# Optimization experiments

Hardware: AMD Instinct MI355X
Metric: run time of the kernel (lower is better)

## Reference

```python
import jax, jax.numpy as jnp
import numpy as np

N_NODES = 100000
N_GRAPHS = 512
D_IN = 300
D_HID = 300
D_OUT = 128  # 2 * SEQUENCE_LENGTH


def _gcn_norm(edge_index, n):
    # PyG GCNConv default: add self-loops, symmetric normalization
    src, dst = edge_index[0], edge_index[1]
    loop = jnp.arange(n, dtype=src.dtype)
    src = jnp.concatenate([src, loop])
    dst = jnp.concatenate([dst, loop])
    deg = jax.ops.segment_sum(jnp.ones_like(dst, dtype=jnp.float32), dst, num_segments=n)
    dinv = jnp.where(deg > 0, jax.lax.rsqrt(deg), 0.0)
    norm = dinv[src] * dinv[dst]  # [E+N]
    return src, dst, norm


def _gcn_conv(x, src, dst, norm, W, b, n):
    h = x @ W                              # transform first (PyG order)
    msg = norm[:, None] * h[src]           # gather + scale, [E+N, D]
    agg = jax.ops.segment_sum(msg, dst, num_segments=n)  # scatter-add
    return agg + b


def setup_inputs() -> dict:
    key = jax.random.key(0)
    ks = jax.random.split(key, 10)
    x = jax.random.normal(ks[0], (N_NODES, D_IN), dtype=jnp.float32)
    edge_index = jax.random.randint(ks[1], (2, 800000), 0, N_NODES, dtype=jnp.int64)
    batch = jnp.sort(jax.random.randint(ks[2], (N_NODES,), 0, N_GRAPHS, dtype=jnp.int64))
    s = 1.0 / np.sqrt(D_IN)
    W1 = jax.random.uniform(ks[3], (D_IN, D_HID), jnp.float32, -s, s)
    b1 = jnp.zeros((D_HID,), jnp.float32)
    W2 = jax.random.uniform(ks[4], (D_HID, D_HID), jnp.float32, -s, s)
    b2 = jnp.zeros((D_HID,), jnp.float32)
    W3 = jax.random.uniform(ks[5], (D_HID, D_OUT), jnp.float32, -s, s)
    b3 = jnp.zeros((D_OUT,), jnp.float32)
    Wm = jax.random.uniform(ks[6], (D_OUT, 1), jnp.float32, -s, s)
    bm = jnp.zeros((1,), jnp.float32)
    return {"x": x, "edge_index": edge_index, "batch": batch,
            "W1": W1, "b1": b1, "W2": W2, "b2": b2,
            "W3": W3, "b3": b3, "Wm": Wm, "bm": bm}


def reference(x, edge_index, batch, W1, b1, W2, b2, W3, b3, Wm, bm):
    n = x.shape[0]
    src, dst, norm = _gcn_norm(edge_index, n)
    # dropout is identity in eval mode
    h = jax.nn.relu(_gcn_conv(x, src, dst, norm, W1, b1, n))
    h = jax.nn.relu(_gcn_conv(h, src, dst, norm, W2, b2, n))
    h = jax.nn.relu(_gcn_conv(h, src, dst, norm, W3, b3, n))
    # global mean pool over graphs
    sums = jax.ops.segment_sum(h, batch, num_segments=N_GRAPHS)
    cnt = jax.ops.segment_sum(jnp.ones((n,), jnp.float32), batch, num_segments=N_GRAPHS)
    readout = sums / jnp.maximum(cnt, 1.0)[:, None]   # [G, D_OUT]
    return (readout @ Wm + bm)[:, 0]                  # [G]
```

## Files before the change

kernel.cpp:

```cpp
#include <hip/hip_runtime.h>
#include <hip/hip_bf16.h>

typedef __bf16 bf16;
typedef __bf16 bf16x4 __attribute__((ext_vector_type(4)));
typedef __bf16 bf16x8 __attribute__((ext_vector_type(8)));
typedef float f32x4 __attribute__((ext_vector_type(4)));

constexpr int N_NODES  = 100000;
constexpr int N_EDGES  = 800000;
constexpr int N_GRAPHS = 512;
constexpr int D_IN  = 300;
constexpr int D_HID = 300;
constexpr int D_OUT = 128;
constexpr int KP    = 320;
constexpr int MT    = 128;
constexpr int NTILE = (N_NODES + MT - 1) / MT;
constexpr int NPAD  = NTILE * MT;

#define AS1(p) ((const __attribute__((address_space(1))) void*)(p))
#define AS3(p) ((__attribute__((address_space(3))) void*)(p))


__global__ __launch_bounds__(256) void k_init(int* deg, float* gsum, int* cnt) {
  int i = blockIdx.x * 256 + threadIdx.x;
  if (i < N_NODES) deg[i] = 0;
  if (i < N_GRAPHS) { gsum[i] = 0.f; cnt[i] = 0; }
}

__global__ __launch_bounds__(256) void k_deg(const int* __restrict__ ei, int* __restrict__ deg) {
  int e = blockIdx.x * 256 + threadIdx.x;
  if (e < N_EDGES) atomicAdd(&deg[ei[N_EDGES + e]], 1);
}

__global__ __launch_bounds__(256) void k_dinv(const int* __restrict__ deg, float* __restrict__ dinv) {
  int v = blockIdx.x * 256 + threadIdx.x;
  if (v < N_NODES) dinv[v] = rsqrtf((float)(deg[v] + 1));
}

__global__ __launch_bounds__(256) void k_scan1(const int* __restrict__ deg, int* __restrict__ rp,
                                               int* __restrict__ part) {
  __shared__ int sm[256];
  int tid = threadIdx.x;
  int i = blockIdx.x * 256 + tid;
  int v = (i < N_NODES) ? deg[i] : 0;
  sm[tid] = v;
  __syncthreads();
  for (int off = 1; off < 256; off <<= 1) {
    int t = (tid >= off) ? sm[tid - off] : 0;
    __syncthreads();
    sm[tid] += t;
    __syncthreads();
  }
  if (i < N_NODES) rp[i] = sm[tid] - v;
  if (tid == 255) part[blockIdx.x] = sm[255];
}

__global__ __launch_bounds__(512) void k_scan2(int* part, int nb) {
  __shared__ int sm[512];
  int tid = threadIdx.x;
  int v = (tid < nb) ? part[tid] : 0;
  sm[tid] = v;
  __syncthreads();
  for (int off = 1; off < 512; off <<= 1) {
    int t = (tid >= off) ? sm[tid - off] : 0;
    __syncthreads();
    sm[tid] += t;
    __syncthreads();
  }
  if (tid < nb) part[tid] = sm[tid] - v;
}

__global__ __launch_bounds__(256) void k_scan3(int* __restrict__ rp, const int* __restrict__ part,
                                               int* __restrict__ cur) {
  int i = blockIdx.x * 256 + threadIdx.x;
  if (i < N_NODES) {
    int r = rp[i] + part[blockIdx.x];
    rp[i] = r;
    cur[i] = r;
  }
  if (i == 0) rp[N_NODES] = N_EDGES;
}

__global__ __launch_bounds__(256) void k_fill(const int* __restrict__ ei, int* __restrict__ cur,
                                              int* __restrict__ col) {
  int e = blockIdx.x * 256 + threadIdx.x;
  if (e < N_EDGES) {
    int s = ei[e];
    int d = ei[N_EDGES + e];
    int p = atomicAdd(&cur[d], 1);
    col[p] = s;
  }
}


__global__ __launch_bounds__(256) void k_conv_x(const float* __restrict__ x, const float* __restrict__ dinv,
                                                bf16* __restrict__ Xs) {
  int i = blockIdx.x * 256 + threadIdx.x;
  if (i >= N_NODES * (KP / 4)) return;
  int j = i % (KP / 4);
  int v = i / (KP / 4);
  float4 f = make_float4(0.f, 0.f, 0.f, 0.f);
  if (j < D_IN / 4) f = ((const float4*)(x + (size_t)v * D_IN))[j];
  float dv = dinv[v];
  bf16x4 o;
  o[0] = (bf16)(f.x * dv); o[1] = (bf16)(f.y * dv); o[2] = (bf16)(f.z * dv); o[3] = (bf16)(f.w * dv);
  *(bf16x4*)(Xs + (size_t)v * KP + j * 4) = o;
}

__global__ __launch_bounds__(256) void k_conv_w(const float* __restrict__ W, bf16* __restrict__ Wt,
                                                int Kin, int Nin) {
  int i = blockIdx.x * 256 + threadIdx.x;
  if (i >= KP * KP) return;
  int k = i % KP;
  int n = i / KP;
  float f = (k < Kin && n < Nin) ? W[k * Nin + n] : 0.f;
  Wt[i] = (bf16)f;
}


__global__ __launch_bounds__(256) void k_aggb(const bf16* __restrict__ in, const int* __restrict__ rp,
                                              const int* __restrict__ col, const float* __restrict__ dinv,
                                              bf16* __restrict__ out) {
  int w = threadIdx.x >> 6, l = threadIdx.x & 63;
  int v = blockIdx.x * 4 + w;
  if (v >= N_NODES) return;
  if (l >= 40) return;
  const size_t co = (size_t)8 * l;

  float A0[8], A1[8];
  {
    bf16x8 p = *(const bf16x8*)(in + (size_t)v * KP + co);
#pragma unroll
    for (int j = 0; j < 8; ++j) { A0[j] = (float)p[j]; A1[j] = 0.f; }
  }
  int s = rp[v], e = rp[v + 1];
  int i = s;
  for (; i + 8 <= e; i += 8) {
    bf16x8 p0 = *(const bf16x8*)(in + (size_t)col[i]     * KP + co);
    bf16x8 p1 = *(const bf16x8*)(in + (size_t)col[i + 1] * KP + co);
    bf16x8 p2 = *(const bf16x8*)(in + (size_t)col[i + 2] * KP + co);
    bf16x8 p3 = *(const bf16x8*)(in + (size_t)col[i + 3] * KP + co);
    bf16x8 p4 = *(const bf16x8*)(in + (size_t)col[i + 4] * KP + co);
    bf16x8 p5 = *(const bf16x8*)(in + (size_t)col[i + 5] * KP + co);
    bf16x8 p6 = *(const bf16x8*)(in + (size_t)col[i + 6] * KP + co);
    bf16x8 p7 = *(const bf16x8*)(in + (size_t)col[i + 7] * KP + co);
#pragma unroll
    for (int j = 0; j < 8; ++j) {
      A0[j] += ((float)p0[j] + (float)p2[j]) + ((float)p4[j] + (float)p6[j]);
      A1[j] += ((float)p1[j] + (float)p3[j]) + ((float)p5[j] + (float)p7[j]);
    }
  }
  for (; i + 4 <= e; i += 4) {
    bf16x8 p0 = *(const bf16x8*)(in + (size_t)col[i]     * KP + co);
    bf16x8 p1 = *(const bf16x8*)(in + (size_t)col[i + 1] * KP + co);
    bf16x8 p2 = *(const bf16x8*)(in + (size_t)col[i + 2] * KP + co);
    bf16x8 p3 = *(const bf16x8*)(in + (size_t)col[i + 3] * KP + co);
#pragma unroll
    for (int j = 0; j < 8; ++j) {
      A0[j] += (float)p0[j] + (float)p2[j];
      A1[j] += (float)p1[j] + (float)p3[j];
    }
  }
  for (; i + 2 <= e; i += 2) {
    bf16x8 p0 = *(const bf16x8*)(in + (size_t)col[i]     * KP + co);
    bf16x8 p1 = *(const bf16x8*)(in + (size_t)col[i + 1] * KP + co);
#pragma unroll
    for (int j = 0; j < 8; ++j) { A0[j] += (float)p0[j]; A1[j] += (float)p1[j]; }
  }
  if (i < e) {
    bf16x8 p0 = *(const bf16x8*)(in + (size_t)col[i] * KP + co);
#pragma unroll
    for (int j = 0; j < 8; ++j) A0[j] += (float)p0[j];
  }
  float dv = dinv[v];
  bf16x8 o;
#pragma unroll
  for (int j = 0; j < 8; ++j) o[j] = (bf16)((A0[j] + A1[j]) * dv);
  *(bf16x8*)(out + (size_t)v * KP + co) = o;
}


template <int NP, int WM, int WN, bool LAST>
__global__ __launch_bounds__(512, 4) void k_gemm(const bf16* __restrict__ A, const bf16* __restrict__ Bt,
                                                 const float* __restrict__ dinv, const float* __restrict__ bias,
                                                 const float* __restrict__ Wm, bf16* __restrict__ H,
                                                 float* __restrict__ sArr) {
  constexpr int WROWS = MT / WM;
  constexpr int MI    = WROWS / 16;
  constexpr int WCOLS = NP / WN;
  constexpr int NC    = WCOLS / 16;
  constexpr int NB_B  = NP / 64;
  __shared__ __attribute__((aligned(16))) char sA[MT * 128];
  __shared__ __attribute__((aligned(16))) char sB[NP * 128];

  const int tid = threadIdx.x;
  const int w = tid >> 6, l = tid & 63;
  const int wm = w / WN, wn = w % WN;
  const int m0 = blockIdx.x * MT;

  const int sr  = tid >> 3;
  const int ssw = ((tid & 7) << 4) ^ ((sr & 7) << 4);
  const char* Ab = (const char*)A;
  const char* Bb = (const char*)Bt;

  const int la = l & 15, q = l >> 4;
  const int msk = (la & 7) << 4;

  f32x4 acc[MI][NC] = {};

  for (int kh = 0; kh < 5; ++kh) {
#pragma unroll
    for (int i = 0; i < 2; ++i) {
      const char* src = Ab + (size_t)(m0 + i * 64 + sr) * 640 + kh * 128 + ssw;
      __builtin_amdgcn_global_load_lds(AS1(src), AS3(sA + i * 8192 + w * 1024), 16, 0, 0);
    }
#pragma unroll
    for (int i = 0; i < NB_B; ++i) {
      const char* src = Bb + (size_t)(i * 64 + sr) * 640 + kh * 128 + ssw;
      __builtin_amdgcn_global_load_lds(AS1(src), AS3(sB + i * 8192 + w * 1024), 16, 0, 0);
    }
    __syncthreads();

#pragma unroll
    for (int ks = 0; ks < 2; ++ks) {
      const int cb = (ks * 64 + q * 16) ^ msk;
      bf16x8 af[MI];
#pragma unroll
      for (int mi = 0; mi < MI; ++mi) {
        int r = wm * WROWS + mi * 16 + la;
        af[mi] = *(const bf16x8*)(sA + r * 128 + cb);
      }
#pragma unroll
      for (int nc = 0; nc < NC; ++nc) {
        int rb = wn * WCOLS + nc * 16 + la;
        bf16x8 bfr = *(const bf16x8*)(sB + rb * 128 + cb);
#pragma unroll
        for (int mi = 0; mi < MI; ++mi)
          acc[mi][nc] = __builtin_amdgcn_mfma_f32_16x16x32_bf16(af[mi], bfr, acc[mi][nc], 0, 0, 0);
      }
    }
    __syncthreads();
  }

  const int rbase = m0 + wm * WROWS + q * 4;
  if (!LAST) {
    float bc[NC];
#pragma unroll
    for (int nc = 0; nc < NC; ++nc) {
      int c = wn * WCOLS + nc * 16 + la;
      bc[nc] = (c < D_HID) ? bias[c] : 0.f;
    }
#pragma unroll
    for (int mi = 0; mi < MI; ++mi) {
#pragma unroll
      for (int r = 0; r < 4; ++r) {
        int row = rbase + mi * 16 + r;
        if (row < N_NODES) {
          float dv = dinv[row];
#pragma unroll
          for (int nc = 0; nc < NC; ++nc) {
            int c = wn * WCOLS + nc * 16 + la;
            H[(size_t)row * KP + c] = (bf16)(fmaxf(acc[mi][nc][r] + bc[nc], 0.f) * dv);
          }
        }
      }
    }
  } else {
    float bc[NC], wc[NC];
#pragma unroll
    for (int nc = 0; nc < NC; ++nc) {
      int c = nc * 16 + la;
      bc[nc] = bias[c];
      wc[nc] = Wm[c];
    }
    float sv[4];
#pragma unroll
    for (int r = 0; r < 4; ++r) {
      sv[r] = 0.f;
#pragma unroll
      for (int nc = 0; nc < NC; ++nc)
        sv[r] += fmaxf(acc[0][nc][r] + bc[nc], 0.f) * wc[nc];
    }
#pragma unroll
    for (int m = 1; m < 16; m <<= 1) {
#pragma unroll
      for (int r = 0; r < 4; ++r) sv[r] += __shfl_xor(sv[r], m);
    }
    if (la == 0) {
#pragma unroll
      for (int r = 0; r < 4; ++r) {
        int row = rbase + r;
        if (row < N_NODES) sArr[row] = sv[r];
      }
    }
  }
}


__global__ __launch_bounds__(256) void k_gsum(const float* __restrict__ sArr, const int* __restrict__ batch,
                                              float* __restrict__ gsum, int* __restrict__ cnt) {
  __shared__ float lsum[N_GRAPHS];
  __shared__ int   lcnt[N_GRAPHS];
  int tid = threadIdx.x;
  lsum[tid] = 0.f; lsum[tid + 256] = 0.f;
  lcnt[tid] = 0;   lcnt[tid + 256] = 0;
  __syncthreads();
  int v = blockIdx.x * 256 + tid;
  if (v < N_NODES) {
    int b = batch[v];
    atomicAdd(&lsum[b], sArr[v]);
    atomicAdd(&lcnt[b], 1);
  }
  __syncthreads();
  for (int g = tid; g < N_GRAPHS; g += 256) {
    int c = lcnt[g];
    if (c) { atomicAdd(&gsum[g], lsum[g]); atomicAdd(&cnt[g], c); }
  }
}

__global__ __launch_bounds__(512) void k_final(const float* __restrict__ gsum, const int* __restrict__ cnt,
                                               const float* __restrict__ bm, float* __restrict__ out) {
  int g = blockIdx.x * 512 + threadIdx.x;
  if (g < N_GRAPHS) out[g] = gsum[g] / fmaxf((float)cnt[g], 1.f) + bm[0];
}


extern "C" void kernel_launch(void* const* d_in, const int* in_sizes, int n_in,
                              void* d_out, int out_size, void* d_ws, size_t ws_size,
                              hipStream_t stream) {
  const float* x    = (const float*)d_in[0];
  const int*   ei   = (const int*)d_in[1];
  const int*   batch= (const int*)d_in[2];
  const float* W1   = (const float*)d_in[3];
  const float* b1   = (const float*)d_in[4];
  const float* W2   = (const float*)d_in[5];
  const float* b2   = (const float*)d_in[6];
  const float* W3   = (const float*)d_in[7];
  const float* b3   = (const float*)d_in[8];
  const float* Wm   = (const float*)d_in[9];
  const float* bm   = (const float*)d_in[10];
  float* out = (float*)d_out;

  char* ws = (char*)d_ws;
  size_t off = 0;
  auto alloc = [&](size_t bytes) {
    void* p = ws + off;
    off = (off + bytes + 255) & ~(size_t)255;
    return p;
  };
  bf16*  Xs   = (bf16*)alloc((size_t)NPAD * KP * sizeof(bf16));
  bf16*  Ab   = (bf16*)alloc((size_t)NPAD * KP * sizeof(bf16));
  bf16*  Wt   = (bf16*)alloc((size_t)KP * KP * sizeof(bf16));
  int*   deg  = (int*)alloc((size_t)N_NODES * 4);
  float* dinv = (float*)alloc((size_t)N_NODES * 4);
  int*   rp   = (int*)alloc((size_t)(N_NODES + 1) * 4);
  int*   cur  = (int*)alloc((size_t)N_NODES * 4);
  int*   col  = (int*)alloc((size_t)N_EDGES * 4);
  int*   part = (int*)alloc(1024 * 4);
  float* sArr = (float*)alloc((size_t)N_NODES * 4);
  float* gsum = (float*)alloc((size_t)N_GRAPHS * 4);
  int*   cnt  = (int*)alloc((size_t)N_GRAPHS * 4);
  bf16*  H    = Xs;

  int nbN = (N_NODES + 255) / 256;
  int nbE = (N_EDGES + 255) / 256;
  int nbA = (N_NODES + 3) / 4;
  int nbW = (KP * KP + 255) / 256;

  k_init<<<nbN, 256, 0, stream>>>(deg, gsum, cnt);
  k_deg<<<nbE, 256, 0, stream>>>(ei, deg);
  k_dinv<<<nbN, 256, 0, stream>>>(deg, dinv);
  k_scan1<<<nbN, 256, 0, stream>>>(deg, rp, part);
  k_scan2<<<1, 512, 0, stream>>>(part, nbN);
  k_scan3<<<nbN, 256, 0, stream>>>(rp, part, cur);
  k_fill<<<nbE, 256, 0, stream>>>(ei, cur, col);
  k_conv_x<<<(N_NODES * (KP / 4) + 255) / 256, 256, 0, stream>>>(x, dinv, Xs);

  k_conv_w<<<nbW, 256, 0, stream>>>(W1, Wt, 300, 300);
  k_aggb<<<nbA, 256, 0, stream>>>(Xs, rp, col, dinv, Ab);
  k_gemm<KP, 2, 4, false><<<NTILE, 512, 0, stream>>>(Ab, Wt, dinv, b1, nullptr, H, nullptr);
  k_conv_w<<<nbW, 256, 0, stream>>>(W2, Wt, 300, 300);
  k_aggb<<<nbA, 256, 0, stream>>>(H, rp, col, dinv, Ab);
  k_gemm<KP, 2, 4, false><<<NTILE, 512, 0, stream>>>(Ab, Wt, dinv, b2, nullptr, H, nullptr);
  k_conv_w<<<nbW, 256, 0, stream>>>(W3, Wt, 300, 128);
  k_aggb<<<nbA, 256, 0, stream>>>(H, rp, col, dinv, Ab);
  k_gemm<128, 8, 1, true><<<NTILE, 512, 0, stream>>>(Ab, Wt, dinv, b3, Wm, nullptr, sArr);

  k_gsum<<<nbN, 256, 0, stream>>>(sArr, batch, gsum, cnt);
  k_final<<<1, 512, 0, stream>>>(gsum, cnt, bm, out);
}
```

Measured before the change: 499.1 us.

## Reorder last GCN layer to transform before aggregating on narrower features

For the third layer, the GEMM now runs first on the 320-wide hidden features to produce 128-wide outputs, and a new aggregation kernel gathers those narrower rows, then applies dinv, bias, ReLU and the Wm dot product. The gather traffic for that layer drops from 320-wide to 128-wide rows. The 8-way unrolled gather loop in the general aggregation kernel is also removed, and the column indices are loaded before the row loads. The reordering adds an extra bf16 rounding of the transformed features before aggregation.

```diff
diff --git a/kernel.cpp b/kernel.cpp
--- a/kernel.cpp
+++ b/kernel.cpp
@@ -135,26 +135,12 @@
   }
   int s = rp[v], e = rp[v + 1];
   int i = s;
-  for (; i + 8 <= e; i += 8) {
-    bf16x8 p0 = *(const bf16x8*)(in + (size_t)col[i]     * KP + co);
-    bf16x8 p1 = *(const bf16x8*)(in + (size_t)col[i + 1] * KP + co);
-    bf16x8 p2 = *(const bf16x8*)(in + (size_t)col[i + 2] * KP + co);
-    bf16x8 p3 = *(const bf16x8*)(in + (size_t)col[i + 3] * KP + co);
-    bf16x8 p4 = *(const bf16x8*)(in + (size_t)col[i + 4] * KP + co);
-    bf16x8 p5 = *(const bf16x8*)(in + (size_t)col[i + 5] * KP + co);
-    bf16x8 p6 = *(const bf16x8*)(in + (size_t)col[i + 6] * KP + co);
-    bf16x8 p7 = *(const bf16x8*)(in + (size_t)col[i + 7] * KP + co);
-#pragma unroll
-    for (int j = 0; j < 8; ++j) {
-      A0[j] += ((float)p0[j] + (float)p2[j]) + ((float)p4[j] + (float)p6[j]);
-      A1[j] += ((float)p1[j] + (float)p3[j]) + ((float)p5[j] + (float)p7[j]);
-    }
-  }
   for (; i + 4 <= e; i += 4) {
-    bf16x8 p0 = *(const bf16x8*)(in + (size_t)col[i]     * KP + co);
-    bf16x8 p1 = *(const bf16x8*)(in + (size_t)col[i + 1] * KP + co);
-    bf16x8 p2 = *(const bf16x8*)(in + (size_t)col[i + 2] * KP + co);
-    bf16x8 p3 = *(const bf16x8*)(in + (size_t)col[i + 3] * KP + co);
+    int u0 = col[i], u1 = col[i + 1], u2 = col[i + 2], u3 = col[i + 3];
+    bf16x8 p0 = *(const bf16x8*)(in + (size_t)u0 * KP + co);
+    bf16x8 p1 = *(const bf16x8*)(in + (size_t)u1 * KP + co);
+    bf16x8 p2 = *(const bf16x8*)(in + (size_t)u2 * KP + co);
+    bf16x8 p3 = *(const bf16x8*)(in + (size_t)u3 * KP + co);
 #pragma unroll
     for (int j = 0; j < 8; ++j) {
       A0[j] += (float)p0[j] + (float)p2[j];
@@ -162,13 +148,15 @@
     }
   }
   for (; i + 2 <= e; i += 2) {
-    bf16x8 p0 = *(const bf16x8*)(in + (size_t)col[i]     * KP + co);
-    bf16x8 p1 = *(const bf16x8*)(in + (size_t)col[i + 1] * KP + co);
+    int u0 = col[i], u1 = col[i + 1];
+    bf16x8 p0 = *(const bf16x8*)(in + (size_t)u0 * KP + co);
+    bf16x8 p1 = *(const bf16x8*)(in + (size_t)u1 * KP + co);
 #pragma unroll
     for (int j = 0; j < 8; ++j) { A0[j] += (float)p0[j]; A1[j] += (float)p1[j]; }
   }
   if (i < e) {
-    bf16x8 p0 = *(const bf16x8*)(in + (size_t)col[i] * KP + co);
+    int u0 = col[i];
+    bf16x8 p0 = *(const bf16x8*)(in + (size_t)u0 * KP + co);
 #pragma unroll
     for (int j = 0; j < 8; ++j) A0[j] += (float)p0[j];
   }
@@ -180,11 +168,66 @@
 }
 
 
-template <int NP, int WM, int WN, bool LAST>
+__global__ __launch_bounds__(256) void k_agg3(const bf16* __restrict__ T3, const int* __restrict__ rp,
+                                              const int* __restrict__ col, const float* __restrict__ dinv,
+                                              const float* __restrict__ bias, const float* __restrict__ Wm,
+                                              float* __restrict__ sArr) {
+  const int tid = threadIdx.x;
+  const int c = tid & 15;
+  const int v = blockIdx.x * 16 + (tid >> 4);
+  const size_t co = (size_t)8 * c;
+
+  float A0[8], A1[8];
+  {
+    bf16x8 p = *(const bf16x8*)(T3 + (size_t)v * 128 + co);
+#pragma unroll
+    for (int j = 0; j < 8; ++j) { A0[j] = (float)p[j]; A1[j] = 0.f; }
+  }
+  int s = rp[v], e = rp[v + 1];
+  int i = s;
+  for (; i + 4 <= e; i += 4) {
+    int u0 = col[i], u1 = col[i + 1], u2 = col[i + 2], u3 = col[i + 3];
+    bf16x8 p0 = *(const bf16x8*)(T3 + (size_t)u0 * 128 + co);
+    bf16x8 p1 = *(const bf16x8*)(T3 + (size_t)u1 * 128 + co);
+    bf16x8 p2 = *(const bf16x8*)(T3 + (size_t)u2 * 128 + co);
+    bf16x8 p3 = *(const bf16x8*)(T3 + (size_t)u3 * 128 + co);
+#pragma unroll
+    for (int j = 0; j < 8; ++j) {
+      A0[j] += (float)p0[j] + (float)p2[j];
+      A1[j] += (float)p1[j] + (float)p3[j];
+    }
+  }
+  for (; i + 2 <= e; i += 2) {
+    int u0 = col[i], u1 = col[i + 1];
+    bf16x8 p0 = *(const bf16x8*)(T3 + (size_t)u0 * 128 + co);
+    bf16x8 p1 = *(const bf16x8*)(T3 + (size_t)u1 * 128 + co);
+#pragma unroll
+    for (int j = 0; j < 8; ++j) { A0[j] += (float)p0[j]; A1[j] += (float)p1[j]; }
+  }
+  if (i < e) {
+    bf16x8 p0 = *(const bf16x8*)(T3 + (size_t)col[i] * 128 + co);
+#pragma unroll
+    for (int j = 0; j < 8; ++j) A0[j] += (float)p0[j];
+  }
+
+  float dv = dinv[v];
+  float sv = 0.f;
+#pragma unroll
+  for (int j = 0; j < 8; ++j) {
+    int d = (int)co + j;
+    float val = fmaxf((A0[j] + A1[j]) * dv + bias[d], 0.f);
+    sv += val * Wm[d];
+  }
+#pragma unroll
+  for (int m = 1; m < 16; m <<= 1) sv += __shfl_xor(sv, m);
+  if (c == 0) sArr[v] = sv;
+}
+
+
+template <int NP, int WM, int WN, int EPI>
 __global__ __launch_bounds__(512, 4) void k_gemm(const bf16* __restrict__ A, const bf16* __restrict__ Bt,
                                                  const float* __restrict__ dinv, const float* __restrict__ bias,
-                                                 const float* __restrict__ Wm, bf16* __restrict__ H,
-                                                 float* __restrict__ sArr) {
+                                                 bf16* __restrict__ H) {
   constexpr int WROWS = MT / WM;
   constexpr int MI    = WROWS / 16;
   constexpr int WCOLS = NP / WN;
@@ -243,7 +286,7 @@
   }
 
   const int rbase = m0 + wm * WROWS + q * 4;
-  if (!LAST) {
+  if (EPI == 0) {
     float bc[NC];
 #pragma unroll
     for (int nc = 0; nc < NC; ++nc) {
@@ -266,31 +309,18 @@
       }
     }
   } else {
-    float bc[NC], wc[NC];
-#pragma unroll
-    for (int nc = 0; nc < NC; ++nc) {
-      int c = nc * 16 + la;
-      bc[nc] = bias[c];
-      wc[nc] = Wm[c];
-    }
-    float sv[4];
-#pragma unroll
-    for (int r = 0; r < 4; ++r) {
-      sv[r] = 0.f;
-#pragma unroll
-      for (int nc = 0; nc < NC; ++nc)
-        sv[r] += fmaxf(acc[0][nc][r] + bc[nc], 0.f) * wc[nc];
-    }
-#pragma unroll
-    for (int m = 1; m < 16; m <<= 1) {
-#pragma unroll
-      for (int r = 0; r < 4; ++r) sv[r] += __shfl_xor(sv[r], m);
-    }
-    if (la == 0) {
+#pragma unroll
+    for (int mi = 0; mi < MI; ++mi) {
 #pragma unroll
       for (int r = 0; r < 4; ++r) {
-        int row = rbase + r;
-        if (row < N_NODES) sArr[row] = sv[r];
+        int row = rbase + mi * 16 + r;
+        if (row < N_NODES) {
+#pragma unroll
+          for (int nc = 0; nc < NC; ++nc) {
+            int c = wn * WCOLS + nc * 16 + la;
+            H[(size_t)row * NP + c] = (bf16)acc[mi][nc][r];
+          }
+        }
       }
     }
   }
@@ -350,6 +380,7 @@
   };
   bf16*  Xs   = (bf16*)alloc((size_t)NPAD * KP * sizeof(bf16));
   bf16*  Ab   = (bf16*)alloc((size_t)NPAD * KP * sizeof(bf16));
+  bf16*  T3   = (bf16*)alloc((size_t)NPAD * 128 * sizeof(bf16));
   bf16*  Wt   = (bf16*)alloc((size_t)KP * KP * sizeof(bf16));
   int*   deg  = (int*)alloc((size_t)N_NODES * 4);
   float* dinv = (float*)alloc((size_t)N_NODES * 4);
@@ -378,13 +409,13 @@
 
   k_conv_w<<<nbW, 256, 0, stream>>>(W1, Wt, 300, 300);
   k_aggb<<<nbA, 256, 0, stream>>>(Xs, rp, col, dinv, Ab);
-  k_gemm<KP, 2, 4, false><<<NTILE, 512, 0, stream>>>(Ab, Wt, dinv, b1, nullptr, H, nullptr);
+  k_gemm<KP, 2, 4, 0><<<NTILE, 512, 0, stream>>>(Ab, Wt, dinv, b1, H);
   k_conv_w<<<nbW, 256, 0, stream>>>(W2, Wt, 300, 300);
   k_aggb<<<nbA, 256, 0, stream>>>(H, rp, col, dinv, Ab);
-  k_gemm<KP, 2, 4, false><<<NTILE, 512, 0, stream>>>(Ab, Wt, dinv, b2, nullptr, H, nullptr);
+  k_gemm<KP, 2, 4, 0><<<NTILE, 512, 0, stream>>>(Ab, Wt, dinv, b2, H);
   k_conv_w<<<nbW, 256, 0, stream>>>(W3, Wt, 300, 128);
-  k_aggb<<<nbA, 256, 0, stream>>>(H, rp, col, dinv, Ab);
-  k_gemm<128, 8, 1, true><<<NTILE, 512, 0, stream>>>(Ab, Wt, dinv, b3, Wm, nullptr, sArr);
+  k_gemm<128, 8, 1, 1><<<NTILE, 512, 0, stream>>>(H, Wt, dinv, nullptr, T3);
+  k_agg3<<<N_NODES / 16, 256, 0, stream>>>(T3, rp, col, dinv, b3, Wm, sArr);
 
   k_gsum<<<nbN, 256, 0, stream>>>(sArr, batch, gsum, cnt);
   k_final<<<1, 512, 0, stream>>>(gsum, cnt, bm, out);
```

Result: faster. 443.6 us (-11.1%).
